# Performance work log

Hardware: AMD Instinct MI355X
Metric: run time of the kernel (lower is better)

Reference implementation:

```python
import jax, jax.numpy as jnp
import numpy as np

VIS_DIM, HID_DIM, ATT_DIM = 1024, 512, 256
B, R = 512, 196


def setup_inputs() -> dict:
    key = jax.random.key(0)
    ks = jax.random.split(key, 8)
    s_v = 1.0 / np.sqrt(VIS_DIM)
    s_h = 1.0 / np.sqrt(HID_DIM)
    s_a = 1.0 / np.sqrt(ATT_DIM)
    return {
        "visual_features": jax.random.normal(ks[0], (B, R, VIS_DIM), jnp.float32),
        "hidden_state": jax.random.normal(ks[1], (B, HID_DIM), jnp.float32),
        "Wv": jax.random.uniform(ks[2], (VIS_DIM, ATT_DIM), jnp.float32, -s_v, s_v),
        "bv": jax.random.uniform(ks[3], (ATT_DIM,), jnp.float32, -s_v, s_v),
        "Wh": jax.random.uniform(ks[4], (HID_DIM, ATT_DIM), jnp.float32, -s_h, s_h),
        "bh": jax.random.uniform(ks[5], (ATT_DIM,), jnp.float32, -s_h, s_h),
        "Wa": jax.random.uniform(ks[6], (ATT_DIM,), jnp.float32, -s_a, s_a),
        "ba": jax.random.uniform(ks[7], (), jnp.float32, -s_a, s_a),
    }


def reference(visual_features, hidden_state, Wv, bv, Wh, bh, Wa, ba):
    # visual_features: [B, R, Dv]; hidden_state: [B, Dh]
    v_proj = jnp.einsum('brd,da->bra', visual_features, Wv) + bv   # [B, R, A]
    h_proj = hidden_state @ Wh + bh                                # [B, A]
    joint = jax.nn.relu(v_proj + h_proj[:, None, :])               # [B, R, A]
    scores = jnp.einsum('bra,a->br', joint, Wa) + ba               # [B, R]
    att = jax.nn.softmax(scores, axis=1)                           # softmax over regions
    att_output = jnp.einsum('br,brd->bd', att, visual_features)    # [B, Dv]
    return att_output
```

## Files before the change

### kernel.cpp

```cpp
#include <hip/hip_runtime.h>
#include <hip/hip_bf16.h>
#include <stdint.h>
#include <stddef.h>

#define BATCH 512
#define RSZ   196
#define DV    1024
#define DH    512
#define DA    256
#define MTOT  (BATCH * RSZ)

typedef short short8 __attribute__((ext_vector_type(8)));
typedef float f32x4 __attribute__((ext_vector_type(4)));

static __device__ __forceinline__ short f2bf(float f) {
    union { float f; unsigned u; } x; x.f = f;
    unsigned r = x.u + 0x7fffu + ((x.u >> 16) & 1u);
    return (short)(r >> 16);
}

static __device__ __forceinline__ int pk2(float x, float y) {
    float2 f; f.x = x; f.y = y;
    __hip_bfloat162 h = __float22bfloat162_rn(f);
    int r; __builtin_memcpy(&r, &h, 4); return r;
}

static __device__ __forceinline__ void gl_lds16(const short* g, short* s) {
    __builtin_amdgcn_global_load_lds(
        (const __attribute__((address_space(1))) void*)g,
        (__attribute__((address_space(3))) void*)s, 16, 0, 0);
}

__global__ __launch_bounds__(256) void k_prep(const float* __restrict__ Wv,
                                              const float* __restrict__ hs,
                                              const float* __restrict__ Wh,
                                              const float* __restrict__ bh,
                                              const float* __restrict__ bv,
                                              short* __restrict__ WvT,
                                              float* __restrict__ H) {
    int tid = threadIdx.x;
    if (blockIdx.x < 64) {
        __shared__ short tile[16][DA];
        int k0 = blockIdx.x * 16;
#pragma unroll
        for (int r = 0; r < 16; ++r)
            tile[r][tid] = f2bf(Wv[(size_t)(k0 + r) * DA + tid]);
        __syncthreads();
        short o[16];
#pragma unroll
        for (int r = 0; r < 16; ++r) o[r] = tile[r][tid];
        *(short8*)&WvT[(size_t)tid * DV + k0]     = *(short8*)&o[0];
        *(short8*)&WvT[(size_t)tid * DV + k0 + 8] = *(short8*)&o[8];
    } else {
        __shared__ float sh[DH];
        int b = blockIdx.x - 64, a = tid;
        sh[a]       = hs[b * DH + a];
        sh[a + 256] = hs[b * DH + 256 + a];
        __syncthreads();
        float acc = 0.f;
#pragma unroll 8
        for (int k = 0; k < DH; ++k) acc += sh[k] * Wh[k * DA + a];
        H[b * DA + a] = acc + bh[a] + bv[a];
    }
}

#define BM  128
#define BN  256
#define BK  64
#define LDA 72

__global__ __launch_bounds__(256, 2) void k_scores(const float* __restrict__ vf,
                                                   const short* __restrict__ WvT,
                                                   const float* __restrict__ H,
                                                   const float* __restrict__ Wa,
                                                   const float* __restrict__ ba,
                                                   float* __restrict__ scores) {
    __shared__ short As[BM * LDA];
    __shared__ short Bs[BN * BK];
    __shared__ float sWa[DA];
    __shared__ float sH[2][DA];
    __shared__ float red[BM][4];

    const int tid = threadIdx.x;
    const int l   = tid & 63;
    const int w   = tid >> 6;
    const int ln  = l & 15;
    const int q   = l >> 4;
    const int m0  = blockIdx.x * BM;
    const int b0  = m0 / RSZ;
    const int bL  = (m0 + BM - 1) / RSZ;

    sWa[tid]   = Wa[tid];
    sH[0][tid] = H[b0 * DA + tid];
    sH[1][tid] = H[bL * DA + tid];

    f32x4 acc[8][4];
#pragma unroll
    for (int i = 0; i < 8; ++i)
#pragma unroll
        for (int j = 0; j < 4; ++j) acc[i][j] = (f32x4){0.f, 0.f, 0.f, 0.f};

    const int ar = tid >> 1;
    const int ac = (tid & 1) * 32;
    const float4* ap = (const float4*)(vf + (size_t)(m0 + ar) * DV + ac);
    short* awr = &As[ar * LDA + ac];

    const int g   = l >> 3;
    const int c   = l & 7;
    const int csw = c ^ g;
    const short* bsrc = WvT + (size_t)(w * 64 + g) * DV + csw * 8;
    short* bdst = &Bs[(w * 8) * 512];

    for (int kt = 0; kt < DV; kt += BK) {
#pragma unroll
        for (int j = 0; j < 8; ++j)
            gl_lds16(bsrc + (size_t)j * 8 * DV + kt, bdst + j * 512);
        int kb = kt >> 2;
        float4 f0 = ap[kb + 0], f1 = ap[kb + 1], f2 = ap[kb + 2], f3 = ap[kb + 3];
        float4 f4 = ap[kb + 4], f5 = ap[kb + 5], f6 = ap[kb + 6], f7 = ap[kb + 7];
        union { short8 v; int i[4]; } u0, u1, u2, u3;
        u0.i[0] = pk2(f0.x, f0.y); u0.i[1] = pk2(f0.z, f0.w);
        u0.i[2] = pk2(f1.x, f1.y); u0.i[3] = pk2(f1.z, f1.w);
        u1.i[0] = pk2(f2.x, f2.y); u1.i[1] = pk2(f2.z, f2.w);
        u1.i[2] = pk2(f3.x, f3.y); u1.i[3] = pk2(f3.z, f3.w);
        u2.i[0] = pk2(f4.x, f4.y); u2.i[1] = pk2(f4.z, f4.w);
        u2.i[2] = pk2(f5.x, f5.y); u2.i[3] = pk2(f5.z, f5.w);
        u3.i[0] = pk2(f6.x, f6.y); u3.i[1] = pk2(f6.z, f6.w);
        u3.i[2] = pk2(f7.x, f7.y); u3.i[3] = pk2(f7.z, f7.w);
        *(short8*)&awr[0]  = u0.v;
        *(short8*)&awr[8]  = u1.v;
        *(short8*)&awr[16] = u2.v;
        *(short8*)&awr[24] = u3.v;
        __syncthreads();
#pragma unroll
        for (int kk = 0; kk < 2; ++kk) {
            short8 bfr[4];
#pragma unroll
            for (int j = 0; j < 4; ++j) {
                int n = w * 64 + j * 16 + ln;
                bfr[j] = *(short8*)&Bs[n * BK + ((4 * kk + q) ^ (ln & 7)) * 8];
            }
#pragma unroll
            for (int i = 0; i < 8; ++i) {
                short8 afr = *(short8*)&As[(i * 16 + ln) * LDA + kk * 32 + q * 8];
#pragma unroll
                for (int j = 0; j < 4; ++j)
                    acc[i][j] = __builtin_amdgcn_mfma_f32_16x16x32_bf16(
                        afr, bfr[j], acc[i][j], 0, 0, 0);
            }
        }
        __syncthreads();
    }

#pragma unroll
    for (int i = 0; i < 8; ++i) {
#pragma unroll
        for (int r = 0; r < 4; ++r) {
            int row = i * 16 + q * 4 + r;
            int bb  = (unsigned)(m0 + row) / RSZ;
            const float* hrow = sH[bb - b0];
            float p = 0.f;
#pragma unroll
            for (int j = 0; j < 4; ++j) {
                int a   = w * 64 + j * 16 + ln;
                float v = acc[i][j][r] + hrow[a];
                p += fmaxf(v, 0.f) * sWa[a];
            }
            p += __shfl_xor(p, 1);
            p += __shfl_xor(p, 2);
            p += __shfl_xor(p, 4);
            p += __shfl_xor(p, 8);
            if (ln == 0) red[row][w] = p;
        }
    }
    __syncthreads();
    if (tid < BM) {
        scores[m0 + tid] = red[tid][0] + red[tid][1] + red[tid][2] + red[tid][3] + ba[0];
    }
}

__global__ __launch_bounds__(256) void k_out(const float* __restrict__ vf,
                                             const float* __restrict__ scores,
                                             float* __restrict__ out) {
    __shared__ float satt[RSZ];
    __shared__ float wrm[4];
    __shared__ float wrs[4];
    const int b = blockIdx.x, t = threadIdx.x;
    const int l = t & 63, w = t >> 6;

    float v = (t < RSZ) ? scores[b * RSZ + t] : -1e30f;
    float m = v;
#pragma unroll
    for (int mk = 32; mk >= 1; mk >>= 1) m = fmaxf(m, __shfl_xor(m, mk));
    if (l == 0) wrm[w] = m;
    __syncthreads();
    m = fmaxf(fmaxf(wrm[0], wrm[1]), fmaxf(wrm[2], wrm[3]));
    float e = (t < RSZ) ? expf(v - m) : 0.f;
    float s = e;
#pragma unroll
    for (int mk = 32; mk >= 1; mk >>= 1) s += __shfl_xor(s, mk);
    if (l == 0) wrs[w] = s;
    __syncthreads();
    s = wrs[0] + wrs[1] + wrs[2] + wrs[3];
    if (t < RSZ) satt[t] = e / s;
    __syncthreads();

    const float4* vp = (const float4*)(vf + (size_t)b * RSZ * DV) + t;
    float4 acc = {0.f, 0.f, 0.f, 0.f};
    for (int r = 0; r < RSZ; r += 4) {
        float4 v0 = vp[(r + 0) * (DV / 4)];
        float4 v1 = vp[(r + 1) * (DV / 4)];
        float4 v2 = vp[(r + 2) * (DV / 4)];
        float4 v3 = vp[(r + 3) * (DV / 4)];
        float a0 = satt[r], a1 = satt[r + 1], a2 = satt[r + 2], a3 = satt[r + 3];
        acc.x += a0 * v0.x + a1 * v1.x + a2 * v2.x + a3 * v3.x;
        acc.y += a0 * v0.y + a1 * v1.y + a2 * v2.y + a3 * v3.y;
        acc.z += a0 * v0.z + a1 * v1.z + a2 * v2.z + a3 * v3.z;
        acc.w += a0 * v0.w + a1 * v1.w + a2 * v2.w + a3 * v3.w;
    }
    ((float4*)(out + (size_t)b * DV))[t] = acc;
}

extern "C" void kernel_launch(void* const* d_in, const int* in_sizes, int n_in,
                              void* d_out, int out_size, void* d_ws, size_t ws_size,
                              hipStream_t stream) {
    const float* vf = (const float*)d_in[0];
    const float* hs = (const float*)d_in[1];
    const float* Wv = (const float*)d_in[2];
    const float* bv = (const float*)d_in[3];
    const float* Wh = (const float*)d_in[4];
    const float* bh = (const float*)d_in[5];
    const float* Wa = (const float*)d_in[6];
    const float* ba = (const float*)d_in[7];
    float* out = (float*)d_out;

    char* ws = (char*)d_ws;
    short* WvT    = (short*)(ws);
    float* H      = (float*)(ws + (512 << 10));
    float* scores = (float*)(ws + (1024 << 10));

    k_prep<<<576, 256, 0, stream>>>(Wv, hs, Wh, bh, bv, WvT, H);
    k_scores<<<MTOT / BM, 256, 0, stream>>>(vf, WvT, H, Wa, ba, scores);
    k_out<<<BATCH, 256, 0, stream>>>(vf, scores, out);
}
```

Before: 695.7 us.

## Fuse score GEMM, softmax and weighted sum into one per-batch kernel

New measurement: 653.2 us. -6.1%, faster.

```diff
diff --git a/kernel.cpp b/kernel.cpp
--- a/kernel.cpp
+++ b/kernel.cpp
@@ -8,7 +8,6 @@
 #define DV    1024
 #define DH    512
 #define DA    256
-#define MTOT  (BATCH * RSZ)
 
 typedef short short8 __attribute__((ext_vector_type(8)));
 typedef float f32x4 __attribute__((ext_vector_type(4)));
@@ -64,46 +63,36 @@
     }
 }
 
-#define BM  128
-#define BN  256
 #define BK  64
 #define LDA 72
 
-__global__ __launch_bounds__(256, 2) void k_scores(const float* __restrict__ vf,
-                                                   const short* __restrict__ WvT,
-                                                   const float* __restrict__ H,
-                                                   const float* __restrict__ Wa,
-                                                   const float* __restrict__ ba,
-                                                   float* __restrict__ scores) {
-    __shared__ short As[BM * LDA];
-    __shared__ short Bs[BN * BK];
+__global__ __launch_bounds__(256, 2) void k_fused(const float* __restrict__ vf,
+                                                  const short* __restrict__ WvT,
+                                                  const float* __restrict__ H,
+                                                  const float* __restrict__ Wa,
+                                                  const float* __restrict__ ba,
+                                                  float* __restrict__ out) {
+    __shared__ short As[64 * LDA];
+    __shared__ short Bs[DA * BK];
+    __shared__ float sH[DA];
     __shared__ float sWa[DA];
-    __shared__ float sH[2][DA];
-    __shared__ float red[BM][4];
+    __shared__ float red[64][4];
+    __shared__ float sp[64];
+    __shared__ float sml[4];
 
     const int tid = threadIdx.x;
     const int l   = tid & 63;
     const int w   = tid >> 6;
     const int ln  = l & 15;
     const int q   = l >> 4;
-    const int m0  = blockIdx.x * BM;
-    const int b0  = m0 / RSZ;
-    const int bL  = (m0 + BM - 1) / RSZ;
-
-    sWa[tid]   = Wa[tid];
-    sH[0][tid] = H[b0 * DA + tid];
-    sH[1][tid] = H[bL * DA + tid];
-
-    f32x4 acc[8][4];
-#pragma unroll
-    for (int i = 0; i < 8; ++i)
-#pragma unroll
-        for (int j = 0; j < 4; ++j) acc[i][j] = (f32x4){0.f, 0.f, 0.f, 0.f};
-
-    const int ar = tid >> 1;
-    const int ac = (tid & 1) * 32;
-    const float4* ap = (const float4*)(vf + (size_t)(m0 + ar) * DV + ac);
-    short* awr = &As[ar * LDA + ac];
+    const int b   = blockIdx.x;
+
+    sH[tid]  = H[b * DA + tid];
+    sWa[tid] = Wa[tid];
+    if (tid == 0) { sml[0] = -1e30f; sml[1] = 0.f; }
+
+    const int ar = tid >> 2;
+    const int ac = (tid & 3) * 16;
 
     const int g   = l >> 3;
     const int c   = l & 7;
@@ -111,114 +100,128 @@
     const short* bsrc = WvT + (size_t)(w * 64 + g) * DV + csw * 8;
     short* bdst = &Bs[(w * 8) * 512];
 
-    for (int kt = 0; kt < DV; kt += BK) {
-#pragma unroll
-        for (int j = 0; j < 8; ++j)
-            gl_lds16(bsrc + (size_t)j * 8 * DV + kt, bdst + j * 512);
-        int kb = kt >> 2;
-        float4 f0 = ap[kb + 0], f1 = ap[kb + 1], f2 = ap[kb + 2], f3 = ap[kb + 3];
-        float4 f4 = ap[kb + 4], f5 = ap[kb + 5], f6 = ap[kb + 6], f7 = ap[kb + 7];
-        union { short8 v; int i[4]; } u0, u1, u2, u3;
-        u0.i[0] = pk2(f0.x, f0.y); u0.i[1] = pk2(f0.z, f0.w);
-        u0.i[2] = pk2(f1.x, f1.y); u0.i[3] = pk2(f1.z, f1.w);
-        u1.i[0] = pk2(f2.x, f2.y); u1.i[1] = pk2(f2.z, f2.w);
-        u1.i[2] = pk2(f3.x, f3.y); u1.i[3] = pk2(f3.z, f3.w);
-        u2.i[0] = pk2(f4.x, f4.y); u2.i[1] = pk2(f4.z, f4.w);
-        u2.i[2] = pk2(f5.x, f5.y); u2.i[3] = pk2(f5.z, f5.w);
-        u3.i[0] = pk2(f6.x, f6.y); u3.i[1] = pk2(f6.z, f6.w);
-        u3.i[2] = pk2(f7.x, f7.y); u3.i[3] = pk2(f7.z, f7.w);
-        *(short8*)&awr[0]  = u0.v;
-        *(short8*)&awr[8]  = u1.v;
-        *(short8*)&awr[16] = u2.v;
-        *(short8*)&awr[24] = u3.v;
-        __syncthreads();
-#pragma unroll
-        for (int kk = 0; kk < 2; ++kk) {
-            short8 bfr[4];
-#pragma unroll
-            for (int j = 0; j < 4; ++j) {
-                int n = w * 64 + j * 16 + ln;
-                bfr[j] = *(short8*)&Bs[n * BK + ((4 * kk + q) ^ (ln & 7)) * 8];
+    float4 O = {0.f, 0.f, 0.f, 0.f};
+    const float baS = ba[0];
+
+    __syncthreads();
+
+    for (int t = 0; t < 4; ++t) {
+        const int r0    = t * 64;
+        const int nrows = (t < 3) ? 64 : (RSZ - 192);
+        const int micnt = (t < 3) ? 4 : 1;
+        const bool rok  = (ar < nrows);
+        const float4* ap = (const float4*)(vf + ((size_t)b * RSZ + r0 + (rok ? ar : 0)) * DV + ac);
+        short* awr = &As[ar * LDA + ac];
+
+        f32x4 acc[4][4];
+#pragma unroll
+        for (int i = 0; i < 4; ++i)
+#pragma unroll
+            for (int j = 0; j < 4; ++j) acc[i][j] = (f32x4){0.f, 0.f, 0.f, 0.f};
+
+        for (int kt = 0; kt < DV; kt += BK) {
+#pragma unroll
+            for (int j = 0; j < 8; ++j)
+                gl_lds16(bsrc + (size_t)j * 8 * DV + kt, bdst + j * 512);
+            int kb = kt >> 2;
+            float4 f0, f1, f2, f3;
+            if (rok) { f0 = ap[kb]; f1 = ap[kb + 1]; f2 = ap[kb + 2]; f3 = ap[kb + 3]; }
+            else     { f0 = f1 = f2 = f3 = (float4){0.f, 0.f, 0.f, 0.f}; }
+            union { short8 v; int i[4]; } u0, u1;
+            u0.i[0] = pk2(f0.x, f0.y); u0.i[1] = pk2(f0.z, f0.w);
+            u0.i[2] = pk2(f1.x, f1.y); u0.i[3] = pk2(f1.z, f1.w);
+            u1.i[0] = pk2(f2.x, f2.y); u1.i[1] = pk2(f2.z, f2.w);
+            u1.i[2] = pk2(f3.x, f3.y); u1.i[3] = pk2(f3.z, f3.w);
+            *(short8*)&awr[0] = u0.v;
+            *(short8*)&awr[8] = u1.v;
+            __syncthreads();
+#pragma unroll
+            for (int kk = 0; kk < 2; ++kk) {
+                short8 bfr[4];
+#pragma unroll
+                for (int j = 0; j < 4; ++j) {
+                    int n = w * 64 + j * 16 + ln;
+                    bfr[j] = *(short8*)&Bs[n * BK + ((4 * kk + q) ^ (ln & 7)) * 8];
+                }
+#pragma unroll
+                for (int i = 0; i < 4; ++i) {
+                    if (i < micnt) {
+                        short8 afr = *(short8*)&As[(i * 16 + ln) * LDA + kk * 32 + q * 8];
+#pragma unroll
+                        for (int j = 0; j < 4; ++j)
+                            acc[i][j] = __builtin_amdgcn_mfma_f32_16x16x32_bf16(
+                                afr, bfr[j], acc[i][j], 0, 0, 0);
+                    }
+                }
             }
-#pragma unroll
-            for (int i = 0; i < 8; ++i) {
-                short8 afr = *(short8*)&As[(i * 16 + ln) * LDA + kk * 32 + q * 8];
-#pragma unroll
-                for (int j = 0; j < 4; ++j)
-                    acc[i][j] = __builtin_amdgcn_mfma_f32_16x16x32_bf16(
-                        afr, bfr[j], acc[i][j], 0, 0, 0);
+            __syncthreads();
+        }
+
+#pragma unroll
+        for (int i = 0; i < 4; ++i) {
+            if (i < micnt) {
+#pragma unroll
+                for (int r = 0; r < 4; ++r) {
+                    int row = i * 16 + q * 4 + r;
+                    float p = 0.f;
+#pragma unroll
+                    for (int j = 0; j < 4; ++j) {
+                        int a   = w * 64 + j * 16 + ln;
+                        float v = acc[i][j][r] + sH[a];
+                        p += fmaxf(v, 0.f) * sWa[a];
+                    }
+                    p += __shfl_xor(p, 1);
+                    p += __shfl_xor(p, 2);
+                    p += __shfl_xor(p, 4);
+                    p += __shfl_xor(p, 8);
+                    if (ln == 0) red[row][w] = p;
+                }
             }
         }
         __syncthreads();
+
+        if (tid < 64) {
+            float s = (tid < nrows)
+                    ? (red[tid][0] + red[tid][1] + red[tid][2] + red[tid][3] + baS)
+                    : -1e30f;
+            float tm = s;
+#pragma unroll
+            for (int mk = 32; mk >= 1; mk >>= 1) tm = fmaxf(tm, __shfl_xor(tm, mk));
+            float m_old = sml[0];
+            float m_new = fmaxf(m_old, tm);
+            float p = (tid < nrows) ? expf(s - m_new) : 0.f;
+            sp[tid] = p;
+            float ls = p;
+#pragma unroll
+            for (int mk = 32; mk >= 1; mk >>= 1) ls += __shfl_xor(ls, mk);
+            if (tid == 0) {
+                float alpha = expf(m_old - m_new);
+                sml[2] = alpha;
+                sml[1] = sml[1] * alpha + ls;
+                sml[0] = m_new;
+            }
+        }
+        __syncthreads();
+
+        float alpha = sml[2];
+        O.x *= alpha; O.y *= alpha; O.z *= alpha; O.w *= alpha;
+        const float4* vrow = (const float4*)(vf + ((size_t)b * RSZ + r0) * DV) + tid;
+        for (int r = 0; r + 3 < nrows; r += 4) {
+            float4 v0 = vrow[(r + 0) * (DV / 4)];
+            float4 v1 = vrow[(r + 1) * (DV / 4)];
+            float4 v2 = vrow[(r + 2) * (DV / 4)];
+            float4 v3 = vrow[(r + 3) * (DV / 4)];
+            float p0 = sp[r], p1 = sp[r + 1], p2 = sp[r + 2], p3 = sp[r + 3];
+            O.x += p0 * v0.x + p1 * v1.x + p2 * v2.x + p3 * v3.x;
+            O.y += p0 * v0.y + p1 * v1.y + p2 * v2.y + p3 * v3.y;
+            O.z += p0 * v0.z + p1 * v1.z + p2 * v2.z + p3 * v3.z;
+            O.w += p0 * v0.w + p1 * v1.w + p2 * v2.w + p3 * v3.w;
+        }
     }
 
-#pragma unroll
-    for (int i = 0; i < 8; ++i) {
-#pragma unroll
-        for (int r = 0; r < 4; ++r) {
-            int row = i * 16 + q * 4 + r;
-            int bb  = (unsigned)(m0 + row) / RSZ;
-            const float* hrow = sH[bb - b0];
-            float p = 0.f;
-#pragma unroll
-            for (int j = 0; j < 4; ++j) {
-                int a   = w * 64 + j * 16 + ln;
-                float v = acc[i][j][r] + hrow[a];
-                p += fmaxf(v, 0.f) * sWa[a];
-            }
-            p += __shfl_xor(p, 1);
-            p += __shfl_xor(p, 2);
-            p += __shfl_xor(p, 4);
-            p += __shfl_xor(p, 8);
-            if (ln == 0) red[row][w] = p;
-        }
-    }
-    __syncthreads();
-    if (tid < BM) {
-        scores[m0 + tid] = red[tid][0] + red[tid][1] + red[tid][2] + red[tid][3] + ba[0];
-    }
-}
-
-__global__ __launch_bounds__(256) void k_out(const float* __restrict__ vf,
-                                             const float* __restrict__ scores,
-                                             float* __restrict__ out) {
-    __shared__ float satt[RSZ];
-    __shared__ float wrm[4];
-    __shared__ float wrs[4];
-    const int b = blockIdx.x, t = threadIdx.x;
-    const int l = t & 63, w = t >> 6;
-
-    float v = (t < RSZ) ? scores[b * RSZ + t] : -1e30f;
-    float m = v;
-#pragma unroll
-    for (int mk = 32; mk >= 1; mk >>= 1) m = fmaxf(m, __shfl_xor(m, mk));
-    if (l == 0) wrm[w] = m;
-    __syncthreads();
-    m = fmaxf(fmaxf(wrm[0], wrm[1]), fmaxf(wrm[2], wrm[3]));
-    float e = (t < RSZ) ? expf(v - m) : 0.f;
-    float s = e;
-#pragma unroll
-    for (int mk = 32; mk >= 1; mk >>= 1) s += __shfl_xor(s, mk);
-    if (l == 0) wrs[w] = s;
-    __syncthreads();
-    s = wrs[0] + wrs[1] + wrs[2] + wrs[3];
-    if (t < RSZ) satt[t] = e / s;
-    __syncthreads();
-
-    const float4* vp = (const float4*)(vf + (size_t)b * RSZ * DV) + t;
-    float4 acc = {0.f, 0.f, 0.f, 0.f};
-    for (int r = 0; r < RSZ; r += 4) {
-        float4 v0 = vp[(r + 0) * (DV / 4)];
-        float4 v1 = vp[(r + 1) * (DV / 4)];
-        float4 v2 = vp[(r + 2) * (DV / 4)];
-        float4 v3 = vp[(r + 3) * (DV / 4)];
-        float a0 = satt[r], a1 = satt[r + 1], a2 = satt[r + 2], a3 = satt[r + 3];
-        acc.x += a0 * v0.x + a1 * v1.x + a2 * v2.x + a3 * v3.x;
-        acc.y += a0 * v0.y + a1 * v1.y + a2 * v2.y + a3 * v3.y;
-        acc.z += a0 * v0.z + a1 * v1.z + a2 * v2.z + a3 * v3.z;
-        acc.w += a0 * v0.w + a1 * v1.w + a2 * v2.w + a3 * v3.w;
-    }
-    ((float4*)(out + (size_t)b * DV))[t] = acc;
+    float invl = 1.f / sml[1];
+    float4 res = {O.x * invl, O.y * invl, O.z * invl, O.w * invl};
+    ((float4*)(out + (size_t)b * DV))[tid] = res;
 }
 
 extern "C" void kernel_launch(void* const* d_in, const int* in_sizes, int n_in,
@@ -235,11 +238,9 @@
     float* out = (float*)d_out;
 
     char* ws = (char*)d_ws;
-    short* WvT    = (short*)(ws);
-    float* H      = (float*)(ws + (512 << 10));
-    float* scores = (float*)(ws + (1024 << 10));
+    short* WvT = (short*)(ws);
+    float* H   = (float*)(ws + (512 << 10));
 
     k_prep<<<576, 256, 0, stream>>>(Wv, hs, Wh, bh, bv, WvT, H);
-    k_scores<<<MTOT / BM, 256, 0, stream>>>(vf, WvT, H, Wa, ba, scores);
-    k_out<<<BATCH, 256, 0, stream>>>(vf, scores, out);
-}
+    k_fused<<<BATCH, 256, 0, stream>>>(vf, WvT, H, Wa, ba, out);
+}
```
